# Kernel tuning notes

Hardware: AMD Instinct MI355X
Metric: run time of the kernel (lower is better)

Reference implementation:

```python
import math
import jax, jax.numpy as jnp
import numpy as np

B, C, T = 4, 512, 1024
H = 8
KC = C // H
WIN = 4


def _get_relative_embeddings(emb, length):
    win = (emb.shape[1] - 1) // 2
    pad_length = max(length - (win + 1), 0)
    slice_start = max(win + 1 - length, 0)
    slice_end = slice_start + 2 * length - 1
    if pad_length > 0:
        emb = jnp.pad(emb, ((0, 0), (pad_length, pad_length), (0, 0)))
    return emb[:, slice_start:slice_end]


def _relative_to_absolute(x):
    # x: [b, h, L, 2L-1] -> [b, h, L, L] via skew trick
    b, h, L, _ = x.shape
    x = jnp.pad(x, ((0, 0), (0, 0), (0, 0), (0, 1)))          # [b,h,L,2L]
    x_flat = x.reshape(b, h, L * 2 * L)
    x_flat = jnp.pad(x_flat, ((0, 0), (0, 0), (0, L - 1)))    # [b,h,(L+1)(2L-1)]
    x_final = x_flat.reshape(b, h, L + 1, 2 * L - 1)
    return x_final[:, :, :L, L - 1:]


def _absolute_to_relative(x):
    # x: [b, h, L, L] -> [b, h, L, 2L-1]
    b, h, L, _ = x.shape
    x = jnp.pad(x, ((0, 0), (0, 0), (0, 0), (0, L - 1)))      # [b,h,L,2L-1]
    x_flat = x.reshape(b, h, L * (2 * L - 1))
    x_flat = jnp.pad(x_flat, ((0, 0), (0, 0), (L, 0)))        # [b,h,2L^2]
    x_final = x_flat.reshape(b, h, L, 2 * L)
    return x_final[:, :, :, 1:]


def setup_inputs() -> dict:
    key = jax.random.key(0)
    ks = jax.random.split(key, 12)
    xavier = math.sqrt(6.0 / (C + C))  # xavier_uniform for [C, C, 1] conv weight
    rel_std = KC ** (-0.5)
    return {
        "x": jax.random.normal(ks[0], (B, C, T), dtype=jnp.float32),
        "wq": jax.random.uniform(ks[1], (C, C), jnp.float32, -xavier, xavier),
        "bq": jnp.zeros((C,), jnp.float32),
        "wk": jax.random.uniform(ks[2], (C, C), jnp.float32, -xavier, xavier),
        "bk": jnp.zeros((C,), jnp.float32),
        "wv": jax.random.uniform(ks[3], (C, C), jnp.float32, -xavier, xavier),
        "bv": jnp.zeros((C,), jnp.float32),
        "wo": jax.random.normal(ks[4], (C, C), jnp.float32) * (1.0 / math.sqrt(C)),
        "bo": jnp.zeros((C,), jnp.float32),
        "emb_rel_k": jax.random.normal(ks[5], (1, 2 * WIN + 1, KC), jnp.float32) * rel_std,
        "emb_rel_v": jax.random.normal(ks[6], (1, 2 * WIN + 1, KC), jnp.float32) * rel_std,
    }


def reference(x, wq, bq, wk, bk, wv, bv, wo, bo, emb_rel_k, emb_rel_v):
    b, c, t = x.shape
    # 1x1 conv == channel matmul
    q = jnp.einsum("oi,bit->bot", wq, x) + bq[:, None]
    k = jnp.einsum("oi,bit->bot", wk, x) + bk[:, None]
    v = jnp.einsum("oi,bit->bot", wv, x) + bv[:, None]
    # [b, H, t, kc]
    q = q.reshape(b, H, KC, t).transpose(0, 1, 3, 2)
    k = k.reshape(b, H, KC, t).transpose(0, 1, 3, 2)
    v = v.reshape(b, H, KC, t).transpose(0, 1, 3, 2)
    inv_sqrt = 1.0 / math.sqrt(KC)
    scores = jnp.einsum("bhtc,bhsc->bhts", q, k) * inv_sqrt
    rel_k = _get_relative_embeddings(emb_rel_k, t)[0]            # [2t-1, kc]
    rel_logits = jnp.einsum("bhtc,rc->bhtr", q, rel_k)           # [b,h,t,2t-1]
    scores = scores + _relative_to_absolute(rel_logits) * inv_sqrt
    p_attn = jax.nn.softmax(scores, axis=-1)
    output = jnp.einsum("bhts,bhsc->bhtc", p_attn, v)
    rel_weights = _absolute_to_relative(p_attn)                  # [b,h,t,2t-1]
    rel_v = _get_relative_embeddings(emb_rel_v, t)[0]            # [2t-1, kc]
    output = output + jnp.einsum("bhtr,rc->bhtc", rel_weights, rel_v)
    output = output.transpose(0, 1, 3, 2).reshape(b, c, t)
    return jnp.einsum("oi,bit->bot", wo, output) + bo[:, None]
```

## Files before the change

### kernel.cpp

```cpp
#include <hip/hip_runtime.h>
#include <hip/hip_bf16.h>

#define Bdim 4
#define Cdim 512
#define Tdim 1024
#define Hn   8
#define KCd  64

#define QK_SCALE 0.18033688011112042f

typedef __attribute__((ext_vector_type(8))) short bf16x8;
typedef __attribute__((ext_vector_type(4))) float f32x4;

__device__ __forceinline__ unsigned short f32_bf16_rne(float f) {
    unsigned u = __float_as_uint(f);
    u += 0x7FFFu + ((u >> 16) & 1u);
    return (unsigned short)(u >> 16);
}
__device__ __forceinline__ float bf16_f32(unsigned short h) {
    return __uint_as_float(((unsigned)h) << 16);
}
__device__ __forceinline__ void split8(const float* f, bf16x8& h8, bf16x8& l8) {
    #pragma unroll
    for (int e = 0; e < 8; ++e) {
        const unsigned short hh = f32_bf16_rne(f[e]);
        h8[e] = (short)hh;
        l8[e] = (short)f32_bf16_rne(f[e] - bf16_f32(hh));
    }
}

__device__ __forceinline__ int sw(int row, int col) {
    return (row << 6) + ((((col >> 3) ^ (row & 7)) << 3) | (col & 7));
}
__device__ __forceinline__ bf16x8 fragld(const unsigned short* a, int row, int kstep, int quad) {
    return *(const bf16x8*)&a[(row << 6) + ((((kstep << 2) | quad) ^ (row & 7)) << 3)];
}


__global__ __launch_bounds__(256) void prep_kernel(
    const float* __restrict__ wq, const float* __restrict__ wk,
    const float* __restrict__ wv, const float* __restrict__ wo,
    const float* __restrict__ x,
    unsigned short* __restrict__ WAhi, unsigned short* __restrict__ WAlo,
    unsigned short* __restrict__ XBhi, unsigned short* __restrict__ XBlo)
{
    const int w = threadIdx.x >> 6, lane = threadIdx.x & 63;
    const int l15 = lane & 15, quad = lane >> 4;
    const int task = blockIdx.x * 4 + w;

    if (task < 2048) {
        const int mtile = task >> 4, kt = task & 15;
        const int sel = mtile >> 5;
        const float* W = sel == 0 ? wq : (sel == 1 ? wk : (sel == 2 ? wv : wo));
        const int row = (mtile & 31) * 16 + l15;
        const float* p = W + (size_t)row * Cdim + kt * 32 + quad * 8;
        float f[8];
        *(float4*)&f[0] = *(const float4*)p;
        *(float4*)&f[4] = *(const float4*)(p + 4);
        bf16x8 h8, l8;
        split8(f, h8, l8);
        const size_t base = (size_t)task * 512 + lane * 8;
        *(bf16x8*)(WAhi + base) = h8;
        *(bf16x8*)(WAlo + base) = l8;
    } else {
        const int t2 = task - 2048;
        const int b = t2 >> 10, ntile = (t2 >> 4) & 63, kt = t2 & 15;
        const float* Xb = x + (size_t)b * Cdim * Tdim;
        const int n = ntile * 16 + l15;
        const int k0 = kt * 32 + quad * 8;
        float f[8];
        #pragma unroll
        for (int e = 0; e < 8; ++e) f[e] = Xb[(size_t)(k0 + e) * Tdim + n];
        bf16x8 h8, l8;
        split8(f, h8, l8);
        const size_t base = (size_t)t2 * 512 + lane * 8;
        *(bf16x8*)(XBhi + base) = h8;
        *(bf16x8*)(XBlo + base) = l8;
    }
}

__global__ __launch_bounds__(256, 3) void gemm_qkv(
    const unsigned short* __restrict__ Ahi, const unsigned short* __restrict__ Alo,
    const unsigned short* __restrict__ Bhi, const unsigned short* __restrict__ Blo,
    const float* __restrict__ bq, const float* __restrict__ bk, const float* __restrict__ bv,
    unsigned short* __restrict__ qhi, unsigned short* __restrict__ qlo,
    unsigned short* __restrict__ khi, unsigned short* __restrict__ klo,
    unsigned short* __restrict__ vhi, unsigned short* __restrict__ vlo)
{
    const int tid = threadIdx.x;
    const int w = tid >> 6, lane = tid & 63;
    const int l15 = lane & 15, quad = lane >> 4;
    const int lo8 = lane << 3;

    const int id = blockIdx.x;
    const int xcd = id & 7, slot = id >> 3;
    const int col = xcd * 16 + slot / 6;
    const int mg  = slot % 6;
    const int b = col >> 5, n32 = col & 31;
    const int m64 = mg * 4 + w;
    const int sel = m64 >> 3;
    const int mtb = m64 * 4;
    const int ntb = b * 64 + n32 * 2;

    f32x4 acc[4][2];
    #pragma unroll
    for (int i = 0; i < 4; ++i)
        #pragma unroll
        for (int j = 0; j < 2; ++j) acc[i][j] = (f32x4){0.f, 0.f, 0.f, 0.f};

    bf16x8 Ah[2][4], Al[2][4], Bh[2][2], Bl[2][2];
    #pragma unroll
    for (int mt = 0; mt < 4; ++mt) {
        const size_t o = (size_t)(mtb + mt) * 8192 + lo8;
        Ah[0][mt] = *(const bf16x8*)(Ahi + o);
        Al[0][mt] = *(const bf16x8*)(Alo + o);
    }
    #pragma unroll
    for (int nt = 0; nt < 2; ++nt) {
        const size_t o = (size_t)(ntb + nt) * 8192 + lo8;
        Bh[0][nt] = *(const bf16x8*)(Bhi + o);
        Bl[0][nt] = *(const bf16x8*)(Blo + o);
    }

    for (int kt = 0; kt < 16; ++kt) {
        const int cur = kt & 1, nxt = cur ^ 1;
        if (kt < 15) {
            const int kn = (kt + 1) * 512;
            #pragma unroll
            for (int mt = 0; mt < 4; ++mt) {
                const size_t o = (size_t)(mtb + mt) * 8192 + kn + lo8;
                Ah[nxt][mt] = *(const bf16x8*)(Ahi + o);
                Al[nxt][mt] = *(const bf16x8*)(Alo + o);
            }
            #pragma unroll
            for (int nt = 0; nt < 2; ++nt) {
                const size_t o = (size_t)(ntb + nt) * 8192 + kn + lo8;
                Bh[nxt][nt] = *(const bf16x8*)(Bhi + o);
                Bl[nxt][nt] = *(const bf16x8*)(Blo + o);
            }
        }
        #pragma unroll
        for (int mt = 0; mt < 4; ++mt)
            #pragma unroll
            for (int nt = 0; nt < 2; ++nt) {
                f32x4 c = acc[mt][nt];
                c = __builtin_amdgcn_mfma_f32_16x16x32_bf16(Ah[cur][mt], Bh[cur][nt], c, 0, 0, 0);
                c = __builtin_amdgcn_mfma_f32_16x16x32_bf16(Ah[cur][mt], Bl[cur][nt], c, 0, 0, 0);
                c = __builtin_amdgcn_mfma_f32_16x16x32_bf16(Al[cur][mt], Bh[cur][nt], c, 0, 0, 0);
                acc[mt][nt] = c;
            }
    }

    const int head = m64 & 7;
    const size_t hbase = ((size_t)(b * Hn + head) * 16) << 12;
    if (sel < 2) {
        const float* Bv = sel == 0 ? bq : bk;
        unsigned short* ph = sel == 0 ? qhi : khi;
        unsigned short* pl = sel == 0 ? qlo : klo;
        const float qscale = sel == 0 ? QK_SCALE : 1.0f;
        #pragma unroll
        for (int mt = 0; mt < 4; ++mt) {
            const int c0 = mt * 16 + quad * 4;
            float bb[4];
            #pragma unroll
            for (int r = 0; r < 4; ++r) bb[r] = Bv[head * 64 + c0 + r];
            const int lane_out = (((c0 >> 3) & 3) << 4) + l15;
            const int e0 = c0 & 7;
            const int cg = c0 >> 5;
            #pragma unroll
            for (int nt = 0; nt < 2; ++nt) {
                const int tile = n32 >> 1;
                const int rhi = (n32 & 1) * 2 + nt;
                const int g = rhi * 2 + cg;
                const size_t off = hbase + ((size_t)tile << 12) + g * 512
                                 + (size_t)lane_out * 8 + e0;
                ushort4 h4, l4;
                #pragma unroll
                for (int r = 0; r < 4; ++r) {
                    const float v = (acc[mt][nt][r] + bb[r]) * qscale;
                    const unsigned short hh = f32_bf16_rne(v);
                    ((unsigned short*)&h4)[r] = hh;
                    ((unsigned short*)&l4)[r] = f32_bf16_rne(v - bf16_f32(hh));
                }
                *(ushort4*)(ph + off) = h4;
                *(ushort4*)(pl + off) = l4;
            }
        }
    } else {
        #pragma unroll
        for (int mt = 0; mt < 4; ++mt) {
            const int c0 = mt * 16 + quad * 4;
            float bb[4];
            #pragma unroll
            for (int r = 0; r < 4; ++r) bb[r] = bv[head * 64 + c0 + r];
            #pragma unroll
            for (int nt = 0; nt < 2; ++nt) {
                const int t = n32 * 32 + nt * 16 + l15;
                const int tile = t >> 6, jl = t & 63;
                const int jg = jl >> 5, lanej = ((jl >> 3) & 3) << 4;
                const int e = jl & 7;
                const size_t tb = hbase + ((size_t)tile << 12);
                #pragma unroll
                for (int r = 0; r < 4; ++r) {
                    const int c = c0 + r;
                    const int g = mt * 2 + jg;
                    const int lane_v = lanej + (c & 15);
                    const float v = acc[mt][nt][r] + bb[r];
                    const unsigned short hh = f32_bf16_rne(v);
                    const size_t off = tb + g * 512 + (size_t)lane_v * 8 + e;
                    vhi[off] = hh;
                    vlo[off] = f32_bf16_rne(v - bf16_f32(hh));
                }
            }
        }
    }
}

__global__ __launch_bounds__(256) void gemm_out(
    const unsigned short* __restrict__ Ahi, const unsigned short* __restrict__ Alo,
    const unsigned short* __restrict__ Bhi, const unsigned short* __restrict__ Blo,
    const float* __restrict__ bo, float* __restrict__ out)
{
    const int tid = threadIdx.x;
    const int w = tid >> 6, lane = tid & 63;
    const int l15 = lane & 15, quad = lane >> 4;
    const int lo8 = lane << 3;

    const int id = blockIdx.x;
    const int xcd = id & 7, slot = id >> 3;
    const int col = xcd * 16 + (slot >> 2);
    const int mg  = slot & 3;
    const int b = col >> 5, n32 = col & 31;
    const int m32 = mg * 4 + w;
    const int mtb = 96 + m32 * 2;
    const int ntb = b * 64 + n32 * 2;

    f32x4 acc[2][2];
    #pragma unroll
    for (int i = 0; i < 2; ++i)
        #pragma unroll
        for (int j = 0; j < 2; ++j) acc[i][j] = (f32x4){0.f, 0.f, 0.f, 0.f};

    bf16x8 Ah[2][2], Al[2][2], Bh[2][2], Bl[2][2];
    #pragma unroll
    for (int mt = 0; mt < 2; ++mt) {
        const size_t o = (size_t)(mtb + mt) * 8192 + lo8;
        Ah[0][mt] = *(const bf16x8*)(Ahi + o);
        Al[0][mt] = *(const bf16x8*)(Alo + o);
    }
    #pragma unroll
    for (int nt = 0; nt < 2; ++nt) {
        const size_t o = (size_t)(ntb + nt) * 8192 + lo8;
        Bh[0][nt] = *(const bf16x8*)(Bhi + o);
        Bl[0][nt] = *(const bf16x8*)(Blo + o);
    }

    for (int kt = 0; kt < 16; ++kt) {
        const int cur = kt & 1, nxt = cur ^ 1;
        if (kt < 15) {
            const int kn = (kt + 1) * 512;
            #pragma unroll
            for (int mt = 0; mt < 2; ++mt) {
                const size_t o = (size_t)(mtb + mt) * 8192 + kn + lo8;
                Ah[nxt][mt] = *(const bf16x8*)(Ahi + o);
                Al[nxt][mt] = *(const bf16x8*)(Alo + o);
            }
            #pragma unroll
            for (int nt = 0; nt < 2; ++nt) {
                const size_t o = (size_t)(ntb + nt) * 8192 + kn + lo8;
                Bh[nxt][nt] = *(const bf16x8*)(Bhi + o);
                Bl[nxt][nt] = *(const bf16x8*)(Blo + o);
            }
        }
        #pragma unroll
        for (int mt = 0; mt < 2; ++mt)
            #pragma unroll
            for (int nt = 0; nt < 2; ++nt) {
                f32x4 c = acc[mt][nt];
                c = __builtin_amdgcn_mfma_f32_16x16x32_bf16(Ah[cur][mt], Bh[cur][nt], c, 0, 0, 0);
                c = __builtin_amdgcn_mfma_f32_16x16x32_bf16(Ah[cur][mt], Bl[cur][nt], c, 0, 0, 0);
                c = __builtin_amdgcn_mfma_f32_16x16x32_bf16(Al[cur][mt], Bh[cur][nt], c, 0, 0, 0);
                acc[mt][nt] = c;
            }
    }

    float* Ob = out + (size_t)b * Cdim * Tdim;
    #pragma unroll
    for (int mt = 0; mt < 2; ++mt) {
        const int m = m32 * 32 + mt * 16 + quad * 4;
        float bb[4];
        #pragma unroll
        for (int r = 0; r < 4; ++r) bb[r] = bo[m + r];
        #pragma unroll
        for (int nt = 0; nt < 2; ++nt) {
            const int t = n32 * 32 + nt * 16 + l15;
            #pragma unroll
            for (int r = 0; r < 4; ++r)
                Ob[(size_t)(m + r) * Tdim + t] = acc[mt][nt][r] + bb[r];
        }
    }
}

__global__ __launch_bounds__(256) void attn_mfma(
    const unsigned short* __restrict__ qhi, const unsigned short* __restrict__ qlo,
    const unsigned short* __restrict__ khi, const unsigned short* __restrict__ klo,
    const unsigned short* __restrict__ vhi, const unsigned short* __restrict__ vlo,
    const float* __restrict__ ek,
    const float* __restrict__ ev,
    unsigned short* __restrict__ cxhi, unsigned short* __restrict__ cxlo)
{
    __shared__ alignas(16) unsigned short psh[4096], psl[4096];
    __shared__ float rk[576];
    __shared__ float evs[576];
    __shared__ float bandp[576];

    const int tid = threadIdx.x;
    int it, h, b;
    {
        const int n = blockIdx.x;
        const int xcd = n & 7, slot = n >> 3;
        const int pair = (xcd << 2) | (slot >> 4);
        it = slot & 15;
        b = pair >> 3;
        h = pair & 7;
    }
    const int i0 = it * 64;
    const int lane = tid & 63, w = tid >> 6;
    const int l15 = lane & 15, quad = lane >> 4;
    const int m_blk = w * 16 + l15;
    const int lo8 = lane << 3;

    const size_t bh16 = (size_t)(b * Hn + h) * 16;

    bf16x8 qfh[2], qfl[2];
    {
        const unsigned short* qth = qhi + ((bh16 + it) << 12);
        const unsigned short* qtl = qlo + ((bh16 + it) << 12);
        #pragma unroll
        for (int ks = 0; ks < 2; ++ks) {
            qfh[ks] = *(const bf16x8*)(qth + (((w << 1) | ks) << 9) + lo8);
            qfl[ks] = *(const bf16x8*)(qtl + (((w << 1) | ks) << 9) + lo8);
        }
    }

    bf16x8 ekh[2], ekl[2];
    #pragma unroll
    for (int ks = 0; ks < 2; ++ks) {
        #pragma unroll
        for (int j = 0; j < 8; ++j) { ekh[ks][j] = 0; ekl[ks][j] = 0; }
        if (l15 < 9) {
            #pragma unroll
            for (int j = 0; j < 8; ++j) {
                const float v = ek[l15 * 64 + ks * 32 + quad * 8 + j];
                const unsigned short hh = f32_bf16_rne(v);
                ekh[ks][j] = (short)hh;
                ekl[ks][j] = (short)f32_bf16_rne(v - bf16_f32(hh));
            }
        }
    }

    {
        f32x4 rkD = (f32x4){0.f, 0.f, 0.f, 0.f};
        #pragma unroll
        for (int ks = 0; ks < 2; ++ks) {
            rkD = __builtin_amdgcn_mfma_f32_16x16x32_bf16(qfh[ks], ekh[ks], rkD, 0, 0, 0);
            rkD = __builtin_amdgcn_mfma_f32_16x16x32_bf16(qfh[ks], ekl[ks], rkD, 0, 0, 0);
            rkD = __builtin_amdgcn_mfma_f32_16x16x32_bf16(qfl[ks], ekh[ks], rkD, 0, 0, 0);
        }
        if (l15 < 9) {
            #pragma unroll
            for (int r = 0; r < 4; ++r)
                rk[(w * 16 + quad * 4 + r) * 9 + l15] = rkD[r];
        }
    }
    for (int idx = tid; idx < 576; idx += 256) evs[idx] = ev[idx];
    __syncthreads();

    float m_run = -1e30f, l_run = 0.f;
    f32x4 Oc[4];
    #pragma unroll
    for (int ct = 0; ct < 4; ++ct) Oc[ct] = (f32x4){0.f, 0.f, 0.f, 0.f};

    const unsigned short* kh0 = khi + (bh16 << 12);
    const unsigned short* kl0 = klo + (bh16 << 12);
    const unsigned short* vh0 = vhi + (bh16 << 12);
    const unsigned short* vl0 = vlo + (bh16 << 12);

    for (int t = 0; t < 16; ++t) {
        const int j0 = t << 6;
        const size_t tb = (size_t)t << 12;
        const unsigned short* kht = kh0 + tb;
        const unsigned short* klt = kl0 + tb;
        const unsigned short* vht = vh0 + tb;
        const unsigned short* vlt = vl0 + tb;

        bf16x8 vbh[2][4], vbl[2][4];
        #pragma unroll
        for (int ks = 0; ks < 2; ++ks)
            #pragma unroll
            for (int ct = 0; ct < 4; ++ct) {
                vbh[ks][ct] = *(const bf16x8*)(vht + (((ct << 1) | ks) << 9) + lo8);
                vbl[ks][ct] = *(const bf16x8*)(vlt + (((ct << 1) | ks) << 9) + lo8);
            }

        f32x4 Sc[4];
        #pragma unroll
        for (int jt = 0; jt < 4; ++jt) Sc[jt] = (f32x4){0.f, 0.f, 0.f, 0.f};
        #pragma unroll
        for (int ks = 0; ks < 2; ++ks) {
            bf16x8 ah[4], al[4];
            #pragma unroll
            for (int jt = 0; jt < 4; ++jt) {
                ah[jt] = *(const bf16x8*)(kht + (((jt << 1) | ks) << 9) + lo8);
                al[jt] = *(const bf16x8*)(klt + (((jt << 1) | ks) << 9) + lo8);
            }
            #pragma unroll
            for (int jt = 0; jt < 4; ++jt) {
                Sc[jt] = __builtin_amdgcn_mfma_f32_16x16x32_bf16(ah[jt], qfh[ks], Sc[jt], 0, 0, 0);
                Sc[jt] = __builtin_amdgcn_mfma_f32_16x16x32_bf16(ah[jt], qfl[ks], Sc[jt], 0, 0, 0);
                Sc[jt] = __builtin_amdgcn_mfma_f32_16x16x32_bf16(al[jt], qfh[ks], Sc[jt], 0, 0, 0);
            }
        }

        const int dt = j0 - i0;
        const bool diag = (dt >= -67 && dt <= 67);
        if (diag) {
            #pragma unroll
            for (int jt = 0; jt < 4; ++jt) {
                const int db = dt + jt * 16 + quad * 4 - m_blk;
                #pragma unroll
                for (int r = 0; r < 4; ++r) {
                    const int d = db + r;
                    if ((unsigned)(d + 4) <= 8u) Sc[jt][r] += rk[m_blk * 9 + d + 4];
                }
            }
        }

        const float mt = fmaxf(
            fmaxf(fmaxf(fmaxf(Sc[0][0], Sc[0][1]), fmaxf(Sc[0][2], Sc[0][3])),
                  fmaxf(fmaxf(Sc[1][0], Sc[1][1]), fmaxf(Sc[1][2], Sc[1][3]))),
            fmaxf(fmaxf(fmaxf(Sc[2][0], Sc[2][1]), fmaxf(Sc[2][2], Sc[2][3])),
                  fmaxf(fmaxf(Sc[3][0], Sc[3][1]), fmaxf(Sc[3][2], Sc[3][3]))));
        float mr = fmaxf(mt, __shfl_xor(mt, 16));
        mr = fmaxf(mr, __shfl_xor(mr, 32));
        const float mn = fmaxf(m_run, mr);
        const float alpha = __builtin_amdgcn_exp2f(m_run - mn);

        #pragma unroll
        for (int jt = 0; jt < 4; ++jt)
            #pragma unroll
            for (int r = 0; r < 4; ++r)
                Sc[jt][r] = __builtin_amdgcn_exp2f(Sc[jt][r] - mn);

        float rs = ((Sc[0][0] + Sc[0][1]) + (Sc[0][2] + Sc[0][3]))
                 + ((Sc[1][0] + Sc[1][1]) + (Sc[1][2] + Sc[1][3]))
                 + ((Sc[2][0] + Sc[2][1]) + (Sc[2][2] + Sc[2][3]))
                 + ((Sc[3][0] + Sc[3][1]) + (Sc[3][2] + Sc[3][3]));
        rs += __shfl_xor(rs, 16);
        rs += __shfl_xor(rs, 32);
        l_run = l_run * alpha + rs;
        m_run = mn;

        if (diag) {
            #pragma unroll
            for (int jt = 0; jt < 4; ++jt) {
                const int db = dt + jt * 16 + quad * 4 - m_blk;
                #pragma unroll
                for (int r = 0; r < 4; ++r) {
                    const int d = db + r;
                    if ((unsigned)(d + 4) <= 8u) bandp[m_blk * 9 + d + 4] = Sc[jt][r];
                }
            }
        }

        #pragma unroll
        for (int jt = 0; jt < 4; ++jt) {
            ushort4 ph, pl;
            ph.x = f32_bf16_rne(Sc[jt][0]); pl.x = f32_bf16_rne(Sc[jt][0] - bf16_f32(ph.x));
            ph.y = f32_bf16_rne(Sc[jt][1]); pl.y = f32_bf16_rne(Sc[jt][1] - bf16_f32(ph.y));
            ph.z = f32_bf16_rne(Sc[jt][2]); pl.z = f32_bf16_rne(Sc[jt][2] - bf16_f32(ph.z));
            ph.w = f32_bf16_rne(Sc[jt][3]); pl.w = f32_bf16_rne(Sc[jt][3] - bf16_f32(ph.w));
            const int o = sw(m_blk, jt * 16 + quad * 4);
            *(ushort4*)&psh[o] = ph;
            *(ushort4*)&psl[o] = pl;
        }

        const float al0 = __shfl(alpha, quad * 4 + 0);
        const float al1 = __shfl(alpha, quad * 4 + 1);
        const float al2 = __shfl(alpha, quad * 4 + 2);
        const float al3 = __shfl(alpha, quad * 4 + 3);
        #pragma unroll
        for (int ct = 0; ct < 4; ++ct) {
            Oc[ct][0] *= al0; Oc[ct][1] *= al1; Oc[ct][2] *= al2; Oc[ct][3] *= al3;
        }
        #pragma unroll
        for (int ks = 0; ks < 2; ++ks) {
            bf16x8 pah = fragld(psh, m_blk, ks, quad);
            bf16x8 pal = fragld(psl, m_blk, ks, quad);
            #pragma unroll
            for (int ct = 0; ct < 4; ++ct) {
                Oc[ct] = __builtin_amdgcn_mfma_f32_16x16x32_bf16(pah, vbh[ks][ct], Oc[ct], 0, 0, 0);
                Oc[ct] = __builtin_amdgcn_mfma_f32_16x16x32_bf16(pah, vbl[ks][ct], Oc[ct], 0, 0, 0);
                Oc[ct] = __builtin_amdgcn_mfma_f32_16x16x32_bf16(pal, vbh[ks][ct], Oc[ct], 0, 0, 0);
            }
        }

        if (diag) {
            #pragma unroll
            for (int r = 0; r < 4; ++r) {
                const int mrow = w * 16 + quad * 4 + r;
                const int ig = i0 + mrow;
                #pragma unroll
                for (int e = 0; e < 9; ++e) {
                    const int jl = ig + e - 4 - j0;
                    if ((unsigned)jl < 64u) {
                        const float p = bandp[mrow * 9 + e];
                        #pragma unroll
                        for (int ct = 0; ct < 4; ++ct)
                            Oc[ct][r] += p * evs[e * 64 + ct * 16 + l15];
                    }
                }
            }
        }
    }

    const float rlv = 1.f / l_run;
    float rl[4];
    rl[0] = __shfl(rlv, quad * 4 + 0);
    rl[1] = __shfl(rlv, quad * 4 + 1);
    rl[2] = __shfl(rlv, quad * 4 + 2);
    rl[3] = __shfl(rlv, quad * 4 + 3);
    const int ntile16 = it * 4 + w;
    const int e = l15 & 7;
    #pragma unroll
    for (int ct = 0; ct < 4; ++ct) {
        const int cl = ct * 16 + l15;
        const int ktc = h * 2 + (cl >> 5);
        const int lane_c = (((ct * 2 + (l15 >> 3)) & 3) << 4) + quad * 4;
        const size_t base = (((size_t)(b * 64 + ntile16)) * 16 + ktc) * 512;
        #pragma unroll
        for (int r = 0; r < 4; ++r) {
            const float v = Oc[ct][r] * rl[r];
            const unsigned short hh = f32_bf16_rne(v);
            const size_t off = base + (size_t)(lane_c + r) * 8 + e;
            cxhi[off] = hh;
            cxlo[off] = f32_bf16_rne(v - bf16_f32(hh));
        }
    }
}

extern "C" void kernel_launch(void* const* d_in, const int* in_sizes, int n_in,
                              void* d_out, int out_size, void* d_ws, size_t ws_size,
                              hipStream_t stream) {
    const float* x  = (const float*)d_in[0];
    const float* wq = (const float*)d_in[1];
    const float* bq = (const float*)d_in[2];
    const float* wk = (const float*)d_in[3];
    const float* bk = (const float*)d_in[4];
    const float* wv = (const float*)d_in[5];
    const float* bv = (const float*)d_in[6];
    const float* wo = (const float*)d_in[7];
    const float* bo = (const float*)d_in[8];
    const float* ek = (const float*)d_in[9];
    const float* ev = (const float*)d_in[10];
    float* out = (float*)d_out;

    const size_t PW = 2048u * 512u;
    const size_t PX = 4u * 1024u * 512u;
    unsigned short* WAhi = (unsigned short*)d_ws;
    unsigned short* WAlo = WAhi + PW;
    unsigned short* XBhi = WAlo + PW;
    unsigned short* XBlo = XBhi + PX;
    unsigned short* qhi  = XBlo + PX;
    unsigned short* qlo  = qhi + PX;
    unsigned short* khi  = qlo + PX;
    unsigned short* klo  = khi + PX;
    unsigned short* vhi  = klo + PX;
    unsigned short* vlo  = vhi + PX;
    unsigned short* cxhi = vlo + PX;
    unsigned short* cxlo = cxhi + PX;

    prep_kernel<<<dim3(1536), 256, 0, stream>>>(
        wq, wk, wv, wo, x, WAhi, WAlo, XBhi, XBlo);

    gemm_qkv<<<dim3(768), 256, 0, stream>>>(
        WAhi, WAlo, XBhi, XBlo, bq, bk, bv,
        qhi, qlo, khi, klo, vhi, vlo);

    attn_mfma<<<dim3(512), 256, 0, stream>>>(
        qhi, qlo, khi, klo, vhi, vlo, ek, ev, cxhi, cxlo);

    gemm_out<<<dim3(512), 256, 0, stream>>>(
        WAhi, WAlo, cxhi, cxlo, bo, out);
}
```

Measured before the change: 185.7 us.

## Split attention KV loop across two wave groups with LDS softmax merge

Doubles the attention block to 512 threads. Each group of four waves processes half of the key/value tiles, and the partial O, max and sum values are then merged flash-decoding style through shared memory. The goal is more parallelism and latency hiding per query tile, because the 512-block grid only gave one block of 4 waves per CU. The cost is extra LDS, a barrier plus merge step, and register pressure under launch_bounds(512,4). The diagonal band and rk setup rely on the split being correct.

Result: slower. 215.9 us (+16.3%).

```diff
diff --git a/kernel.cpp b/kernel.cpp
--- a/kernel.cpp
+++ b/kernel.cpp
@@ -301,7 +301,7 @@
     }
 }
 
-__global__ __launch_bounds__(256) void attn_mfma(
+__global__ __launch_bounds__(512, 4) void attn_mfma(
     const unsigned short* __restrict__ qhi, const unsigned short* __restrict__ qlo,
     const unsigned short* __restrict__ khi, const unsigned short* __restrict__ klo,
     const unsigned short* __restrict__ vhi, const unsigned short* __restrict__ vlo,
@@ -309,10 +309,12 @@
     const float* __restrict__ ev,
     unsigned short* __restrict__ cxhi, unsigned short* __restrict__ cxlo)
 {
-    __shared__ alignas(16) unsigned short psh[4096], psl[4096];
+    __shared__ alignas(16) unsigned short psh[2][4096], psl[2][4096];
     __shared__ float rk[576];
     __shared__ float evs[576];
-    __shared__ float bandp[576];
+    __shared__ float bandp[2][576];
+    __shared__ float mO[4][16][64];
+    __shared__ float mML[4][2][64];
 
     const int tid = threadIdx.x;
     int it, h, b;
@@ -326,9 +328,15 @@
     }
     const int i0 = it * 64;
     const int lane = tid & 63, w = tid >> 6;
+    const int s = w >> 2;
+    const int w4 = w & 3;
     const int l15 = lane & 15, quad = lane >> 4;
-    const int m_blk = w * 16 + l15;
+    const int m_blk = w4 * 16 + l15;
     const int lo8 = lane << 3;
+
+    unsigned short* pshS = psh[s];
+    unsigned short* pslS = psl[s];
+    float* bandS = bandp[s];
 
     const size_t bh16 = (size_t)(b * Hn + h) * 16;
 
@@ -338,28 +346,27 @@
         const unsigned short* qtl = qlo + ((bh16 + it) << 12);
         #pragma unroll
         for (int ks = 0; ks < 2; ++ks) {
-            qfh[ks] = *(const bf16x8*)(qth + (((w << 1) | ks) << 9) + lo8);
-            qfl[ks] = *(const bf16x8*)(qtl + (((w << 1) | ks) << 9) + lo8);
-        }
-    }
-
-    bf16x8 ekh[2], ekl[2];
-    #pragma unroll
-    for (int ks = 0; ks < 2; ++ks) {
-        #pragma unroll
-        for (int j = 0; j < 8; ++j) { ekh[ks][j] = 0; ekl[ks][j] = 0; }
-        if (l15 < 9) {
-            #pragma unroll
-            for (int j = 0; j < 8; ++j) {
-                const float v = ek[l15 * 64 + ks * 32 + quad * 8 + j];
-                const unsigned short hh = f32_bf16_rne(v);
-                ekh[ks][j] = (short)hh;
-                ekl[ks][j] = (short)f32_bf16_rne(v - bf16_f32(hh));
-            }
-        }
-    }
-
-    {
+            qfh[ks] = *(const bf16x8*)(qth + (((w4 << 1) | ks) << 9) + lo8);
+            qfl[ks] = *(const bf16x8*)(qtl + (((w4 << 1) | ks) << 9) + lo8);
+        }
+    }
+
+    if (s == 0) {
+        bf16x8 ekh[2], ekl[2];
+        #pragma unroll
+        for (int ks = 0; ks < 2; ++ks) {
+            #pragma unroll
+            for (int j = 0; j < 8; ++j) { ekh[ks][j] = 0; ekl[ks][j] = 0; }
+            if (l15 < 9) {
+                #pragma unroll
+                for (int j = 0; j < 8; ++j) {
+                    const float v = ek[l15 * 64 + ks * 32 + quad * 8 + j];
+                    const unsigned short hh = f32_bf16_rne(v);
+                    ekh[ks][j] = (short)hh;
+                    ekl[ks][j] = (short)f32_bf16_rne(v - bf16_f32(hh));
+                }
+            }
+        }
         f32x4 rkD = (f32x4){0.f, 0.f, 0.f, 0.f};
         #pragma unroll
         for (int ks = 0; ks < 2; ++ks) {
@@ -370,10 +377,10 @@
         if (l15 < 9) {
             #pragma unroll
             for (int r = 0; r < 4; ++r)
-                rk[(w * 16 + quad * 4 + r) * 9 + l15] = rkD[r];
-        }
-    }
-    for (int idx = tid; idx < 576; idx += 256) evs[idx] = ev[idx];
+                rk[(w4 * 16 + quad * 4 + r) * 9 + l15] = rkD[r];
+        }
+    }
+    for (int idx = tid; idx < 576; idx += 512) evs[idx] = ev[idx];
     __syncthreads();
 
     float m_run = -1e30f, l_run = 0.f;
@@ -386,7 +393,8 @@
     const unsigned short* vh0 = vhi + (bh16 << 12);
     const unsigned short* vl0 = vlo + (bh16 << 12);
 
-    for (int t = 0; t < 16; ++t) {
+    for (int tt = 0; tt < 8; ++tt) {
+        const int t = (s << 3) + tt;
         const int j0 = t << 6;
         const size_t tb = (size_t)t << 12;
         const unsigned short* kht = kh0 + tb;
@@ -468,7 +476,7 @@
                 #pragma unroll
                 for (int r = 0; r < 4; ++r) {
                     const int d = db + r;
-                    if ((unsigned)(d + 4) <= 8u) bandp[m_blk * 9 + d + 4] = Sc[jt][r];
+                    if ((unsigned)(d + 4) <= 8u) bandS[m_blk * 9 + d + 4] = Sc[jt][r];
                 }
             }
         }
@@ -481,8 +489,8 @@
             ph.z = f32_bf16_rne(Sc[jt][2]); pl.z = f32_bf16_rne(Sc[jt][2] - bf16_f32(ph.z));
             ph.w = f32_bf16_rne(Sc[jt][3]); pl.w = f32_bf16_rne(Sc[jt][3] - bf16_f32(ph.w));
             const int o = sw(m_blk, jt * 16 + quad * 4);
-            *(ushort4*)&psh[o] = ph;
-            *(ushort4*)&psl[o] = pl;
+            *(ushort4*)&pshS[o] = ph;
+            *(ushort4*)&pslS[o] = pl;
         }
 
         const float al0 = __shfl(alpha, quad * 4 + 0);
@@ -495,8 +503,8 @@
         }
         #pragma unroll
         for (int ks = 0; ks < 2; ++ks) {
-            bf16x8 pah = fragld(psh, m_blk, ks, quad);
-            bf16x8 pal = fragld(psl, m_blk, ks, quad);
+            bf16x8 pah = fragld(pshS, m_blk, ks, quad);
+            bf16x8 pal = fragld(pslS, m_blk, ks, quad);
             #pragma unroll
             for (int ct = 0; ct < 4; ++ct) {
                 Oc[ct] = __builtin_amdgcn_mfma_f32_16x16x32_bf16(pah, vbh[ks][ct], Oc[ct], 0, 0, 0);
@@ -508,13 +516,13 @@
         if (diag) {
             #pragma unroll
             for (int r = 0; r < 4; ++r) {
-                const int mrow = w * 16 + quad * 4 + r;
+                const int mrow = w4 * 16 + quad * 4 + r;
                 const int ig = i0 + mrow;
                 #pragma unroll
                 for (int e = 0; e < 9; ++e) {
                     const int jl = ig + e - 4 - j0;
                     if ((unsigned)jl < 64u) {
-                        const float p = bandp[mrow * 9 + e];
+                        const float p = bandS[mrow * 9 + e];
                         #pragma unroll
                         for (int ct = 0; ct < 4; ++ct)
                             Oc[ct][r] += p * evs[e * 64 + ct * 16 + l15];
@@ -524,13 +532,34 @@
         }
     }
 
-    const float rlv = 1.f / l_run;
-    float rl[4];
-    rl[0] = __shfl(rlv, quad * 4 + 0);
-    rl[1] = __shfl(rlv, quad * 4 + 1);
-    rl[2] = __shfl(rlv, quad * 4 + 2);
-    rl[3] = __shfl(rlv, quad * 4 + 3);
-    const int ntile16 = it * 4 + w;
+    if (s == 1) {
+        #pragma unroll
+        for (int ct = 0; ct < 4; ++ct)
+            #pragma unroll
+            for (int r = 0; r < 4; ++r)
+                mO[w4][ct * 4 + r][lane] = Oc[ct][r];
+        mML[w4][0][lane] = m_run;
+        mML[w4][1][lane] = l_run;
+    }
+    __syncthreads();
+    if (s == 1) return;
+
+    const float m1 = mML[w4][0][lane];
+    const float l1 = mML[w4][1][lane];
+    const float mm = fmaxf(m_run, m1);
+    const float a0 = __builtin_amdgcn_exp2f(m_run - mm);
+    const float a1 = __builtin_amdgcn_exp2f(m1 - mm);
+    const float rlv = 1.f / (l_run * a0 + l1 * a1);
+
+    float a0r[4], a1r[4], rl[4];
+    #pragma unroll
+    for (int r = 0; r < 4; ++r) {
+        a0r[r] = __shfl(a0, quad * 4 + r);
+        a1r[r] = __shfl(a1, quad * 4 + r);
+        rl[r]  = __shfl(rlv, quad * 4 + r);
+    }
+
+    const int ntile16 = it * 4 + w4;
     const int e = l15 & 7;
     #pragma unroll
     for (int ct = 0; ct < 4; ++ct) {
@@ -540,7 +569,7 @@
         const size_t base = (((size_t)(b * 64 + ntile16)) * 16 + ktc) * 512;
         #pragma unroll
         for (int r = 0; r < 4; ++r) {
-            const float v = Oc[ct][r] * rl[r];
+            const float v = (Oc[ct][r] * a0r[r] + mO[w4][ct * 4 + r][lane] * a1r[r]) * rl[r];
             const unsigned short hh = f32_bf16_rne(v);
             const size_t off = base + (size_t)(lane_c + r) * 8 + e;
             cxhi[off] = hh;
@@ -587,7 +616,7 @@
         WAhi, WAlo, XBhi, XBlo, bq, bk, bv,
         qhi, qlo, khi, klo, vhi, vlo);
 
-    attn_mfma<<<dim3(512), 256, 0, stream>>>(
+    attn_mfma<<<dim3(512), 512, 0, stream>>>(
         qhi, qlo, khi, klo, vhi, vlo, ek, ev, cxhi, cxlo);
 
     gemm_out<<<dim3(512), 256, 0, stream>>>(
```

## Prefetch next K tile into registers and raise MFMA wave priority

Applied to the files above, without the earlier changes.

Each attention tile now loads the first k-slice of the next tile's K fragments into a ping-pong register set while the current tile computes. The loop is unrolled by two through a lambda so the buffers swap without copies. s_setprio is raised around the MFMA blocks so waves doing matrix work get issue priority. This is meant to hide global-load latency for K, at the cost of more VGPRs and possibly lower occupancy.

Result: slower. 191.8 us (+3.3%).

```diff
diff --git a/kernel.cpp b/kernel.cpp
--- a/kernel.cpp
+++ b/kernel.cpp
@@ -343,6 +343,18 @@
         }
     }
 
+    const unsigned short* kh0 = khi + (bh16 << 12);
+    const unsigned short* kl0 = klo + (bh16 << 12);
+    const unsigned short* vh0 = vhi + (bh16 << 12);
+    const unsigned short* vl0 = vlo + (bh16 << 12);
+
+    bf16x8 kAh[4], kAl[4], kBh[4], kBl[4];
+    #pragma unroll
+    for (int jt = 0; jt < 4; ++jt) {
+        kAh[jt] = *(const bf16x8*)(kh0 + ((jt << 1) << 9) + lo8);
+        kAl[jt] = *(const bf16x8*)(kl0 + ((jt << 1) << 9) + lo8);
+    }
+
     bf16x8 ekh[2], ekl[2];
     #pragma unroll
     for (int ks = 0; ks < 2; ++ks) {
@@ -381,12 +393,8 @@
     #pragma unroll
     for (int ct = 0; ct < 4; ++ct) Oc[ct] = (f32x4){0.f, 0.f, 0.f, 0.f};
 
-    const unsigned short* kh0 = khi + (bh16 << 12);
-    const unsigned short* kl0 = klo + (bh16 << 12);
-    const unsigned short* vh0 = vhi + (bh16 << 12);
-    const unsigned short* vl0 = vlo + (bh16 << 12);
-
-    for (int t = 0; t < 16; ++t) {
+    auto tile_step = [&](int t, bf16x8 (&kch)[4], bf16x8 (&kcl)[4],
+                         bf16x8 (&knh)[4], bf16x8 (&knl)[4], bool pf) {
         const int j0 = t << 6;
         const size_t tb = (size_t)t << 12;
         const unsigned short* kht = kh0 + tb;
@@ -402,25 +410,37 @@
                 vbh[ks][ct] = *(const bf16x8*)(vht + (((ct << 1) | ks) << 9) + lo8);
                 vbl[ks][ct] = *(const bf16x8*)(vlt + (((ct << 1) | ks) << 9) + lo8);
             }
+        bf16x8 a1h[4], a1l[4];
+        #pragma unroll
+        for (int jt = 0; jt < 4; ++jt) {
+            a1h[jt] = *(const bf16x8*)(kht + (((jt << 1) | 1) << 9) + lo8);
+            a1l[jt] = *(const bf16x8*)(klt + (((jt << 1) | 1) << 9) + lo8);
+        }
+        if (pf) {
+            #pragma unroll
+            for (int jt = 0; jt < 4; ++jt) {
+                knh[jt] = *(const bf16x8*)(kht + 4096 + ((jt << 1) << 9) + lo8);
+                knl[jt] = *(const bf16x8*)(klt + 4096 + ((jt << 1) << 9) + lo8);
+            }
+        }
 
         f32x4 Sc[4];
         #pragma unroll
         for (int jt = 0; jt < 4; ++jt) Sc[jt] = (f32x4){0.f, 0.f, 0.f, 0.f};
-        #pragma unroll
-        for (int ks = 0; ks < 2; ++ks) {
-            bf16x8 ah[4], al[4];
-            #pragma unroll
-            for (int jt = 0; jt < 4; ++jt) {
-                ah[jt] = *(const bf16x8*)(kht + (((jt << 1) | ks) << 9) + lo8);
-                al[jt] = *(const bf16x8*)(klt + (((jt << 1) | ks) << 9) + lo8);
-            }
-            #pragma unroll
-            for (int jt = 0; jt < 4; ++jt) {
-                Sc[jt] = __builtin_amdgcn_mfma_f32_16x16x32_bf16(ah[jt], qfh[ks], Sc[jt], 0, 0, 0);
-                Sc[jt] = __builtin_amdgcn_mfma_f32_16x16x32_bf16(ah[jt], qfl[ks], Sc[jt], 0, 0, 0);
-                Sc[jt] = __builtin_amdgcn_mfma_f32_16x16x32_bf16(al[jt], qfh[ks], Sc[jt], 0, 0, 0);
-            }
-        }
+        __builtin_amdgcn_s_setprio(1);
+        #pragma unroll
+        for (int jt = 0; jt < 4; ++jt) {
+            Sc[jt] = __builtin_amdgcn_mfma_f32_16x16x32_bf16(kch[jt], qfh[0], Sc[jt], 0, 0, 0);
+            Sc[jt] = __builtin_amdgcn_mfma_f32_16x16x32_bf16(kch[jt], qfl[0], Sc[jt], 0, 0, 0);
+            Sc[jt] = __builtin_amdgcn_mfma_f32_16x16x32_bf16(kcl[jt], qfh[0], Sc[jt], 0, 0, 0);
+        }
+        #pragma unroll
+        for (int jt = 0; jt < 4; ++jt) {
+            Sc[jt] = __builtin_amdgcn_mfma_f32_16x16x32_bf16(a1h[jt], qfh[1], Sc[jt], 0, 0, 0);
+            Sc[jt] = __builtin_amdgcn_mfma_f32_16x16x32_bf16(a1h[jt], qfl[1], Sc[jt], 0, 0, 0);
+            Sc[jt] = __builtin_amdgcn_mfma_f32_16x16x32_bf16(a1l[jt], qfh[1], Sc[jt], 0, 0, 0);
+        }
+        __builtin_amdgcn_s_setprio(0);
 
         const int dt = j0 - i0;
         const bool diag = (dt >= -67 && dt <= 67);
@@ -493,6 +513,7 @@
         for (int ct = 0; ct < 4; ++ct) {
             Oc[ct][0] *= al0; Oc[ct][1] *= al1; Oc[ct][2] *= al2; Oc[ct][3] *= al3;
         }
+        __builtin_amdgcn_s_setprio(1);
         #pragma unroll
         for (int ks = 0; ks < 2; ++ks) {
             bf16x8 pah = fragld(psh, m_blk, ks, quad);
@@ -504,6 +525,7 @@
                 Oc[ct] = __builtin_amdgcn_mfma_f32_16x16x32_bf16(pal, vbh[ks][ct], Oc[ct], 0, 0, 0);
             }
         }
+        __builtin_amdgcn_s_setprio(0);
 
         if (diag) {
             #pragma unroll
@@ -522,6 +544,12 @@
                 }
             }
         }
+    };
+
+    #pragma unroll 1
+    for (int t2 = 0; t2 < 16; t2 += 2) {
+        tile_step(t2,     kAh, kAl, kBh, kBl, true);
+        tile_step(t2 + 1, kBh, kBl, kAh, kAl, t2 + 2 < 16);
     }
 
     const float rlv = 1.f / l_run;
```

## Share GEMM operand tiles across waves via double-buffered LDS staging

Applied to the files above, without the earlier changes.

In the QKV projection kernel, block-to-tile mapping is changed so that the four waves in a block share the same weight rows and differ in output column. Each wave loads one quarter of the shared A tile (hi/lo split) into a double-buffered LDS array instead of every wave loading all four rows from global memory. The output GEMM does the same for its B operand, with each wave staging one of the hi/lo halves. This is meant to cut redundant global/L2 traffic, at the cost of LDS reads and a per-iteration block barrier.

Result: faster. 162.1 us (-12.7%).

```diff
diff --git a/kernel.cpp b/kernel.cpp
--- a/kernel.cpp
+++ b/kernel.cpp
@@ -87,6 +87,8 @@
     unsigned short* __restrict__ khi, unsigned short* __restrict__ klo,
     unsigned short* __restrict__ vhi, unsigned short* __restrict__ vlo)
 {
+    __shared__ alignas(16) unsigned short As[2][4][2][512];
+
     const int tid = threadIdx.x;
     const int w = tid >> 6, lane = tid & 63;
     const int l15 = lane & 15, quad = lane >> 4;
@@ -94,44 +96,41 @@
 
     const int id = blockIdx.x;
     const int xcd = id & 7, slot = id >> 3;
-    const int col = xcd * 16 + slot / 6;
-    const int mg  = slot % 6;
+    const int m64 = slot >> 2;
+    const int col128 = xcd * 4 + (slot & 3);
+    const int col = col128 * 4 + w;
     const int b = col >> 5, n32 = col & 31;
-    const int m64 = mg * 4 + w;
     const int sel = m64 >> 3;
     const int mtb = m64 * 4;
     const int ntb = b * 64 + n32 * 2;
 
+    const unsigned short* Asrc_h = Ahi + (size_t)(mtb + w) * 8192 + lo8;
+    const unsigned short* Asrc_l = Alo + (size_t)(mtb + w) * 8192 + lo8;
+
     f32x4 acc[4][2];
     #pragma unroll
     for (int i = 0; i < 4; ++i)
         #pragma unroll
         for (int j = 0; j < 2; ++j) acc[i][j] = (f32x4){0.f, 0.f, 0.f, 0.f};
 
-    bf16x8 Ah[2][4], Al[2][4], Bh[2][2], Bl[2][2];
-    #pragma unroll
-    for (int mt = 0; mt < 4; ++mt) {
-        const size_t o = (size_t)(mtb + mt) * 8192 + lo8;
-        Ah[0][mt] = *(const bf16x8*)(Ahi + o);
-        Al[0][mt] = *(const bf16x8*)(Alo + o);
-    }
+    bf16x8 Bh[2][2], Bl[2][2];
     #pragma unroll
     for (int nt = 0; nt < 2; ++nt) {
         const size_t o = (size_t)(ntb + nt) * 8192 + lo8;
         Bh[0][nt] = *(const bf16x8*)(Bhi + o);
         Bl[0][nt] = *(const bf16x8*)(Blo + o);
     }
+    *(bf16x8*)&As[0][w][0][lo8] = *(const bf16x8*)Asrc_h;
+    *(bf16x8*)&As[0][w][1][lo8] = *(const bf16x8*)Asrc_l;
+    __syncthreads();
 
     for (int kt = 0; kt < 16; ++kt) {
         const int cur = kt & 1, nxt = cur ^ 1;
+        bf16x8 stgh, stgl;
         if (kt < 15) {
             const int kn = (kt + 1) * 512;
-            #pragma unroll
-            for (int mt = 0; mt < 4; ++mt) {
-                const size_t o = (size_t)(mtb + mt) * 8192 + kn + lo8;
-                Ah[nxt][mt] = *(const bf16x8*)(Ahi + o);
-                Al[nxt][mt] = *(const bf16x8*)(Alo + o);
-            }
+            stgh = *(const bf16x8*)(Asrc_h + kn);
+            stgl = *(const bf16x8*)(Asrc_l + kn);
             #pragma unroll
             for (int nt = 0; nt < 2; ++nt) {
                 const size_t o = (size_t)(ntb + nt) * 8192 + kn + lo8;
@@ -139,16 +138,27 @@
                 Bl[nxt][nt] = *(const bf16x8*)(Blo + o);
             }
         }
+        bf16x8 Afh[4], Afl[4];
+        #pragma unroll
+        for (int mt = 0; mt < 4; ++mt) {
+            Afh[mt] = *(const bf16x8*)&As[cur][mt][0][lo8];
+            Afl[mt] = *(const bf16x8*)&As[cur][mt][1][lo8];
+        }
         #pragma unroll
         for (int mt = 0; mt < 4; ++mt)
             #pragma unroll
             for (int nt = 0; nt < 2; ++nt) {
                 f32x4 c = acc[mt][nt];
-                c = __builtin_amdgcn_mfma_f32_16x16x32_bf16(Ah[cur][mt], Bh[cur][nt], c, 0, 0, 0);
-                c = __builtin_amdgcn_mfma_f32_16x16x32_bf16(Ah[cur][mt], Bl[cur][nt], c, 0, 0, 0);
-                c = __builtin_amdgcn_mfma_f32_16x16x32_bf16(Al[cur][mt], Bh[cur][nt], c, 0, 0, 0);
+                c = __builtin_amdgcn_mfma_f32_16x16x32_bf16(Afh[mt], Bh[cur][nt], c, 0, 0, 0);
+                c = __builtin_amdgcn_mfma_f32_16x16x32_bf16(Afh[mt], Bl[cur][nt], c, 0, 0, 0);
+                c = __builtin_amdgcn_mfma_f32_16x16x32_bf16(Afl[mt], Bh[cur][nt], c, 0, 0, 0);
                 acc[mt][nt] = c;
             }
+        if (kt < 15) {
+            *(bf16x8*)&As[nxt][w][0][lo8] = stgh;
+            *(bf16x8*)&As[nxt][w][1][lo8] = stgl;
+        }
+        __syncthreads();
     }
 
     const int head = m64 & 7;
@@ -221,6 +231,8 @@
     const unsigned short* __restrict__ Bhi, const unsigned short* __restrict__ Blo,
     const float* __restrict__ bo, float* __restrict__ out)
 {
+    __shared__ alignas(16) unsigned short Bs[2][2][2][512];
+
     const int tid = threadIdx.x;
     const int w = tid >> 6, lane = tid & 63;
     const int l15 = lane & 15, quad = lane >> 4;
@@ -235,53 +247,58 @@
     const int mtb = 96 + m32 * 2;
     const int ntb = b * 64 + n32 * 2;
 
+    const unsigned short* Bsrc =
+        ((w & 1) ? Blo : Bhi) + (size_t)(ntb + (w >> 1)) * 8192 + lo8;
+
     f32x4 acc[2][2];
     #pragma unroll
     for (int i = 0; i < 2; ++i)
         #pragma unroll
         for (int j = 0; j < 2; ++j) acc[i][j] = (f32x4){0.f, 0.f, 0.f, 0.f};
 
-    bf16x8 Ah[2][2], Al[2][2], Bh[2][2], Bl[2][2];
+    bf16x8 Ah[2][2], Al[2][2];
     #pragma unroll
     for (int mt = 0; mt < 2; ++mt) {
         const size_t o = (size_t)(mtb + mt) * 8192 + lo8;
         Ah[0][mt] = *(const bf16x8*)(Ahi + o);
         Al[0][mt] = *(const bf16x8*)(Alo + o);
     }
-    #pragma unroll
-    for (int nt = 0; nt < 2; ++nt) {
-        const size_t o = (size_t)(ntb + nt) * 8192 + lo8;
-        Bh[0][nt] = *(const bf16x8*)(Bhi + o);
-        Bl[0][nt] = *(const bf16x8*)(Blo + o);
-    }
+    *(bf16x8*)&Bs[0][w >> 1][w & 1][lo8] = *(const bf16x8*)Bsrc;
+    __syncthreads();
 
     for (int kt = 0; kt < 16; ++kt) {
         const int cur = kt & 1, nxt = cur ^ 1;
+        bf16x8 stg;
         if (kt < 15) {
             const int kn = (kt + 1) * 512;
+            stg = *(const bf16x8*)(Bsrc + kn);
             #pragma unroll
             for (int mt = 0; mt < 2; ++mt) {
                 const size_t o = (size_t)(mtb + mt) * 8192 + kn + lo8;
                 Ah[nxt][mt] = *(const bf16x8*)(Ahi + o);
                 Al[nxt][mt] = *(const bf16x8*)(Alo + o);
             }
-            #pragma unroll
-            for (int nt = 0; nt < 2; ++nt) {
-                const size_t o = (size_t)(ntb + nt) * 8192 + kn + lo8;
-                Bh[nxt][nt] = *(const bf16x8*)(Bhi + o);
-                Bl[nxt][nt] = *(const bf16x8*)(Blo + o);
-            }
+        }
+        bf16x8 Bfh[2], Bfl[2];
+        #pragma unroll
+        for (int nt = 0; nt < 2; ++nt) {
+            Bfh[nt] = *(const bf16x8*)&Bs[cur][nt][0][lo8];
+            Bfl[nt] = *(const bf16x8*)&Bs[cur][nt][1][lo8];
         }
         #pragma unroll
         for (int mt = 0; mt < 2; ++mt)
             #pragma unroll
             for (int nt = 0; nt < 2; ++nt) {
                 f32x4 c = acc[mt][nt];
-                c = __builtin_amdgcn_mfma_f32_16x16x32_bf16(Ah[cur][mt], Bh[cur][nt], c, 0, 0, 0);
-                c = __builtin_amdgcn_mfma_f32_16x16x32_bf16(Ah[cur][mt], Bl[cur][nt], c, 0, 0, 0);
-                c = __builtin_amdgcn_mfma_f32_16x16x32_bf16(Al[cur][mt], Bh[cur][nt], c, 0, 0, 0);
+                c = __builtin_amdgcn_mfma_f32_16x16x32_bf16(Ah[cur][mt], Bfh[nt], c, 0, 0, 0);
+                c = __builtin_amdgcn_mfma_f32_16x16x32_bf16(Ah[cur][mt], Bfl[nt], c, 0, 0, 0);
+                c = __builtin_amdgcn_mfma_f32_16x16x32_bf16(Al[cur][mt], Bfh[nt], c, 0, 0, 0);
                 acc[mt][nt] = c;
             }
+        if (kt < 15) {
+            *(bf16x8*)&Bs[nxt][w >> 1][w & 1][lo8] = stg;
+        }
+        __syncthreads();
     }
 
     float* Ob = out + (size_t)b * Cdim * Tdim;
```
